# Kernel tuning notes

Measured on AMD Instinct MI355X. Metric: run time of the kernel, lower is better.

Reference implementation:

```python
import jax, jax.numpy as jnp
import numpy as np

DIM = 1024
NUM_HEADS = 8
DIM_HEAD = 64
K_NEIGHBORS = 64
INNER = NUM_HEADS * DIM_HEAD
SCALE = DIM_HEAD ** -0.5


def setup_inputs() -> dict:
    key = jax.random.key(0)
    kx, kq, kk = jax.random.split(key, 3)
    x = jax.random.normal(kx, (2, 2048, DIM), dtype=jnp.float32)
    # nn.Linear(dim, inner_dim, bias=False): weight applied as x @ W.T; store as [dim, inner]
    Wq = jax.random.normal(kq, (DIM, INNER), dtype=jnp.float32) * (DIM ** -0.5)
    Wk = jax.random.normal(kk, (DIM, INNER), dtype=jnp.float32) * (DIM ** -0.5)
    return {"x": x, "Wq": Wq, "Wk": Wk}


def reference(x, Wq, Wk):
    b, n, _ = x.shape
    # project and split heads: (b, n, inner) -> (b, h, n, d)
    q = (x @ Wq).reshape(b, n, NUM_HEADS, DIM_HEAD).transpose(0, 2, 1, 3)
    k = (x @ Wk).reshape(b, n, NUM_HEADS, DIM_HEAD).transpose(0, 2, 1, 3)
    scores = jnp.einsum("bhqd,bhkd->bhqk", q, k) * SCALE
    if K_NEIGHBORS < n:
        top_vals, _ = jax.lax.top_k(scores, K_NEIGHBORS)  # (b,h,n,k)
        min_k = top_vals[..., -1:]  # k-th largest per row
        scores = jnp.where(scores < min_k, -jnp.inf, scores)
    return jax.nn.softmax(scores, axis=-1)
```

## Files before the change

### kernel.cpp

```cpp
#include <hip/hip_runtime.h>
#include <math.h>

#define BATCH 2
#define SEQ   2048
#define DIMIN 1024
#define NHEAD 8
#define DHEAD 64
#define INNER 512
#define KNEI  64
#define SCALE 0.125f
#define GBAND 2e-6f

__global__ __launch_bounds__(256) void proj_kernel(
    const float* __restrict__ x, const float* __restrict__ Wq,
    const float* __restrict__ Wk, float* __restrict__ qk)
{
  const int which = blockIdx.z;
  const float* __restrict__ W = which ? Wk : Wq;
  float* __restrict__ out = qk + (size_t)which * (4096ull * (size_t)INNER);
  const int m0 = blockIdx.y * 64;
  const int n0 = blockIdx.x * 64;
  __shared__ float aT[16][68];
  __shared__ float bS[16][68];
  const int t  = threadIdx.x;
  const int ty = t >> 4, tx = t & 15;
  float acc[4][4] = {};
  for (int k0 = 0; k0 < DIMIN; k0 += 16) {
    {
      const int m = t >> 2, c4 = t & 3;
      float4 av = *(const float4*)(x + (size_t)(m0 + m) * DIMIN + k0 + c4 * 4);
      aT[c4*4+0][m] = av.x; aT[c4*4+1][m] = av.y;
      aT[c4*4+2][m] = av.z; aT[c4*4+3][m] = av.w;
    }
    {
      const int kk = t >> 6, n = t & 63;
      #pragma unroll
      for (int s5 = 0; s5 < 4; ++s5)
        bS[kk + 4*s5][n] = W[(size_t)(k0 + kk + 4*s5) * INNER + n0 + n];
    }
    __syncthreads();
    #pragma unroll 4
    for (int kk = 0; kk < 16; ++kk) {
      float4 a4 = *(const float4*)&aT[kk][ty*4];
      float4 b4 = *(const float4*)&bS[kk][tx*4];
      float a[4] = {a4.x, a4.y, a4.z, a4.w};
      float b[4] = {b4.x, b4.y, b4.z, b4.w};
      #pragma unroll
      for (int i = 0; i < 4; ++i)
        #pragma unroll
        for (int j = 0; j < 4; ++j)
          acc[i][j] = fmaf(a[i], b[j], acc[i][j]);
    }
    __syncthreads();
  }
  #pragma unroll
  for (int i = 0; i < 4; ++i) {
    float4 v = make_float4(acc[i][0], acc[i][1], acc[i][2], acc[i][3]);
    *(float4*)(out + (size_t)(m0 + ty*4 + i) * INNER + n0 + tx*4) = v;
  }
}

__global__ __launch_bounds__(256) void score_kernel(
    const float* __restrict__ qk, float* __restrict__ out)
{
  const int bh = blockIdx.z;
  const int b  = bh >> 3, h = bh & 7;
  const int m0 = blockIdx.y * 64;
  const int n0 = blockIdx.x * 64;
  const float* __restrict__ q = qk;
  const float* __restrict__ k = qk + 4096ull * (size_t)INNER;
  __shared__ float qT[64][68];
  __shared__ float kT[64][68];
  const int t = threadIdx.x;
  {
    const int m = t >> 2, dv = t & 3;
    const float* qrow = q + (size_t)(b*SEQ + m0 + m) * INNER + h*DHEAD;
    const float* krow = k + (size_t)(b*SEQ + n0 + m) * INNER + h*DHEAD;
    #pragma unroll
    for (int s5 = 0; s5 < 4; ++s5) {
      const int d0 = (dv + 4*s5) * 4;
      float4 qv = *(const float4*)(qrow + d0);
      float4 kv = *(const float4*)(krow + d0);
      qT[d0+0][m] = qv.x; qT[d0+1][m] = qv.y; qT[d0+2][m] = qv.z; qT[d0+3][m] = qv.w;
      kT[d0+0][m] = kv.x; kT[d0+1][m] = kv.y; kT[d0+2][m] = kv.z; kT[d0+3][m] = kv.w;
    }
  }
  __syncthreads();
  const int ty = t >> 4, tx = t & 15;
  float acc[4][4] = {};
  #pragma unroll 8
  for (int kk = 0; kk < 64; ++kk) {
    float4 a4 = *(const float4*)&qT[kk][ty*4];
    float4 b4 = *(const float4*)&kT[kk][tx*4];
    float a[4] = {a4.x, a4.y, a4.z, a4.w};
    float b[4] = {b4.x, b4.y, b4.z, b4.w};
    #pragma unroll
    for (int i = 0; i < 4; ++i)
      #pragma unroll
      for (int j = 0; j < 4; ++j)
        acc[i][j] = fmaf(a[i], b[j], acc[i][j]);
  }
  #pragma unroll
  for (int i = 0; i < 4; ++i) {
    float4 v = make_float4(acc[i][0]*SCALE, acc[i][1]*SCALE,
                           acc[i][2]*SCALE, acc[i][3]*SCALE);
    *(float4*)(out + ((size_t)bh * SEQ + m0 + ty*4 + i) * SEQ + n0 + tx*4) = v;
  }
}

__device__ __forceinline__ unsigned f2key(float f) {
  unsigned u = __float_as_uint(f);
  return (u & 0x80000000u) ? ~u : (u | 0x80000000u);
}
__device__ __forceinline__ float key2f(unsigned kk) {
  unsigned u = (kk & 0x80000000u) ? (kk & 0x7FFFFFFFu) : ~kk;
  return __uint_as_float(u);
}

__global__ __launch_bounds__(256) void topk_softmax_hedge(float* __restrict__ out)
{
  const int wave = threadIdx.x >> 6;
  const int lane = threadIdx.x & 63;
  const size_t row = (size_t)blockIdx.x * 4 + wave;
  float* __restrict__ p = out + row * (size_t)SEQ;

  float s[32];
  #pragma unroll
  for (int i = 0; i < 8; ++i) {
    float4 v = *(const float4*)(p + (size_t)(lane + 64*i) * 4);
    s[i*4+0] = v.x; s[i*4+1] = v.y; s[i*4+2] = v.z; s[i*4+3] = v.w;
  }

  float mx = s[0], mn = s[0];
  #pragma unroll
  for (int i = 1; i < 32; ++i) { mx = fmaxf(mx, s[i]); mn = fminf(mn, s[i]); }
  #pragma unroll
  for (int o = 32; o; o >>= 1) {
    mx = fmaxf(mx, __shfl_xor(mx, o));
    mn = fminf(mn, __shfl_xor(mn, o));
  }

  unsigned lo = f2key(mn);
  unsigned hi = f2key(mx) + 1u;
  while (lo + 1u < hi) {
    const unsigned mid = lo + ((hi - lo) >> 1);
    const float tf = key2f(mid);
    int c = 0;
    #pragma unroll
    for (int i = 0; i < 32; ++i)
      c += __popcll(__ballot(s[i] >= tf));
    if (c >= KNEI) { lo = mid; if (c == KNEI) break; }
    else hi = mid;
  }
  const float thr0 = key2f(lo);

  float mk = 3.4e38f;
  #pragma unroll
  for (int i = 0; i < 32; ++i) mk = (s[i] >= thr0) ? fminf(mk, s[i]) : mk;
  #pragma unroll
  for (int o = 32; o; o >>= 1) mk = fminf(mk, __shfl_xor(mk, o));
  const float s64 = mk;

  int n_hi = 0, n_band = 0;
  #pragma unroll
  for (int i = 0; i < 32; ++i) {
    n_hi   += __popcll(__ballot(s[i] > s64 + GBAND));
    n_band += __popcll(__ballot(fabsf(s[i] - s64) <= GBAND));
  }
  const int r = KNEI - n_hi;
  const bool amb = (n_band != r);
  float fb = (float)r / (float)max(n_band, 1);
  fb = fminf(fmaxf(fb, 0.f), 1.f);

  float z = 0.f;
  #pragma unroll
  for (int i = 0; i < 32; ++i) {
    float f;
    if (amb) {
      f = (s[i] > s64 + GBAND) ? 1.f
        : ((fabsf(s[i] - s64) <= GBAND) ? fb : 0.f);
    } else {
      f = (s[i] >= s64) ? 1.f : 0.f;
    }
    float ex = f * __expf(s[i] - mx);
    s[i] = ex; z += ex;
  }
  #pragma unroll
  for (int o = 32; o; o >>= 1) z += __shfl_xor(z, o);
  const float rz = 1.0f / z;

  #pragma unroll
  for (int i = 0; i < 8; ++i) {
    float4 v = make_float4(s[i*4+0]*rz, s[i*4+1]*rz, s[i*4+2]*rz, s[i*4+3]*rz);
    *(float4*)(p + (size_t)(lane + 64*i) * 4) = v;
  }
}

extern "C" void kernel_launch(void* const* d_in, const int* in_sizes, int n_in,
                              void* d_out, int out_size, void* d_ws, size_t ws_size,
                              hipStream_t stream) {
  const float* x  = (const float*)d_in[0];
  const float* Wq = (const float*)d_in[1];
  const float* Wk = (const float*)d_in[2];
  float* out = (float*)d_out;
  float* ws  = (float*)d_ws;

  proj_kernel<<<dim3(INNER/64, (BATCH*SEQ)/64, 2), 256, 0, stream>>>(x, Wq, Wk, ws);
  score_kernel<<<dim3(SEQ/64, SEQ/64, BATCH*NHEAD), 256, 0, stream>>>(ws, out);
  topk_softmax_hedge<<<dim3((BATCH*NHEAD*SEQ)/4), 256, 0, stream>>>(out);
}
```

Measured before the change: 355.1 us.

## Fuse score GEMM with top-k softmax so scores stay in registers

Merges the score kernel and the top-k/softmax kernel into one. Each block computes a 16-query by 2048-key score tile, holding the scores in 128 registers per thread, and runs the threshold search and masked softmax directly on them. This removes one write and one read of the 2048x2048 score matrix per head, and the final output uses nontemporal stores. In exchange the register pressure is high (acc[4][32]), which may lower occupancy or cause spills. The K tile is reloaded with less reuse per block than the 64x64 tiling had.

```diff
diff --git a/kernel.cpp b/kernel.cpp
--- a/kernel.cpp
+++ b/kernel.cpp
@@ -60,54 +60,6 @@
   }
 }
 
-__global__ __launch_bounds__(256) void score_kernel(
-    const float* __restrict__ qk, float* __restrict__ out)
-{
-  const int bh = blockIdx.z;
-  const int b  = bh >> 3, h = bh & 7;
-  const int m0 = blockIdx.y * 64;
-  const int n0 = blockIdx.x * 64;
-  const float* __restrict__ q = qk;
-  const float* __restrict__ k = qk + 4096ull * (size_t)INNER;
-  __shared__ float qT[64][68];
-  __shared__ float kT[64][68];
-  const int t = threadIdx.x;
-  {
-    const int m = t >> 2, dv = t & 3;
-    const float* qrow = q + (size_t)(b*SEQ + m0 + m) * INNER + h*DHEAD;
-    const float* krow = k + (size_t)(b*SEQ + n0 + m) * INNER + h*DHEAD;
-    #pragma unroll
-    for (int s5 = 0; s5 < 4; ++s5) {
-      const int d0 = (dv + 4*s5) * 4;
-      float4 qv = *(const float4*)(qrow + d0);
-      float4 kv = *(const float4*)(krow + d0);
-      qT[d0+0][m] = qv.x; qT[d0+1][m] = qv.y; qT[d0+2][m] = qv.z; qT[d0+3][m] = qv.w;
-      kT[d0+0][m] = kv.x; kT[d0+1][m] = kv.y; kT[d0+2][m] = kv.z; kT[d0+3][m] = kv.w;
-    }
-  }
-  __syncthreads();
-  const int ty = t >> 4, tx = t & 15;
-  float acc[4][4] = {};
-  #pragma unroll 8
-  for (int kk = 0; kk < 64; ++kk) {
-    float4 a4 = *(const float4*)&qT[kk][ty*4];
-    float4 b4 = *(const float4*)&kT[kk][tx*4];
-    float a[4] = {a4.x, a4.y, a4.z, a4.w};
-    float b[4] = {b4.x, b4.y, b4.z, b4.w};
-    #pragma unroll
-    for (int i = 0; i < 4; ++i)
-      #pragma unroll
-      for (int j = 0; j < 4; ++j)
-        acc[i][j] = fmaf(a[i], b[j], acc[i][j]);
-  }
-  #pragma unroll
-  for (int i = 0; i < 4; ++i) {
-    float4 v = make_float4(acc[i][0]*SCALE, acc[i][1]*SCALE,
-                           acc[i][2]*SCALE, acc[i][3]*SCALE);
-    *(float4*)(out + ((size_t)bh * SEQ + m0 + ty*4 + i) * SEQ + n0 + tx*4) = v;
-  }
-}
-
 __device__ __forceinline__ unsigned f2key(float f) {
   unsigned u = __float_as_uint(f);
   return (u & 0x80000000u) ? ~u : (u | 0x80000000u);
@@ -117,82 +69,138 @@
   return __uint_as_float(u);
 }
 
-__global__ __launch_bounds__(256) void topk_softmax_hedge(float* __restrict__ out)
+__global__ __launch_bounds__(256) void score_topk_fused(
+    const float* __restrict__ qk, float* __restrict__ out)
 {
-  const int wave = threadIdx.x >> 6;
-  const int lane = threadIdx.x & 63;
-  const size_t row = (size_t)blockIdx.x * 4 + wave;
-  float* __restrict__ p = out + row * (size_t)SEQ;
-
-  float s[32];
-  #pragma unroll
-  for (int i = 0; i < 8; ++i) {
-    float4 v = *(const float4*)(p + (size_t)(lane + 64*i) * 4);
-    s[i*4+0] = v.x; s[i*4+1] = v.y; s[i*4+2] = v.z; s[i*4+3] = v.w;
-  }
-
-  float mx = s[0], mn = s[0];
-  #pragma unroll
-  for (int i = 1; i < 32; ++i) { mx = fmaxf(mx, s[i]); mn = fminf(mn, s[i]); }
-  #pragma unroll
-  for (int o = 32; o; o >>= 1) {
-    mx = fmaxf(mx, __shfl_xor(mx, o));
-    mn = fminf(mn, __shfl_xor(mn, o));
-  }
-
-  unsigned lo = f2key(mn);
-  unsigned hi = f2key(mx) + 1u;
-  while (lo + 1u < hi) {
-    const unsigned mid = lo + ((hi - lo) >> 1);
-    const float tf = key2f(mid);
-    int c = 0;
+  const int bh = blockIdx.y, b = bh >> 3, h = bh & 7;
+  const int q0 = blockIdx.x * 16;
+  const int t = threadIdx.x, lane = t & 63;
+  const int myrow = (t >> 6) * 4;
+  const float* __restrict__ qws = qk;
+  const float* __restrict__ kws = qk + 4096ull * (size_t)INNER;
+
+  __shared__ float kT[64][66];
+  __shared__ float qT[16][68];
+
+  {
+    const int r = t >> 4, dd = (t & 15) * 4;
+    float4 v = *(const float4*)(qws + (size_t)(b*SEQ + q0 + r) * INNER + h*DHEAD + dd);
+    *(float4*)&qT[r][dd] = v;
+  }
+
+  float acc[4][32];
+  #pragma unroll
+  for (int r = 0; r < 4; ++r)
+    #pragma unroll
+    for (int c = 0; c < 32; ++c) acc[r][c] = 0.f;
+
+  const int kt = t >> 2, ds = (t & 3) * 16;
+  const float* kstage = kws + (size_t)(b*SEQ + kt) * INNER + h*DHEAD + ds;
+
+  #pragma unroll
+  for (int c = 0; c < 32; ++c) {
+    __syncthreads();
+    {
+      const float* src = kstage + (size_t)(c*64) * INNER;
+      float4 v0 = *(const float4*)(src);
+      float4 v1 = *(const float4*)(src + 4);
+      float4 v2 = *(const float4*)(src + 8);
+      float4 v3 = *(const float4*)(src + 12);
+      *(float2*)&kT[kt][ds+ 0] = make_float2(v0.x, v0.y);
+      *(float2*)&kT[kt][ds+ 2] = make_float2(v0.z, v0.w);
+      *(float2*)&kT[kt][ds+ 4] = make_float2(v1.x, v1.y);
+      *(float2*)&kT[kt][ds+ 6] = make_float2(v1.z, v1.w);
+      *(float2*)&kT[kt][ds+ 8] = make_float2(v2.x, v2.y);
+      *(float2*)&kT[kt][ds+10] = make_float2(v2.z, v2.w);
+      *(float2*)&kT[kt][ds+12] = make_float2(v3.x, v3.y);
+      *(float2*)&kT[kt][ds+14] = make_float2(v3.z, v3.w);
+    }
+    __syncthreads();
+    #pragma unroll
+    for (int d4 = 0; d4 < 16; ++d4) {
+      float2 k0 = *(const float2*)&kT[lane][d4*4];
+      float2 k1 = *(const float2*)&kT[lane][d4*4+2];
+      #pragma unroll
+      for (int r = 0; r < 4; ++r) {
+        float4 qv = *(const float4*)&qT[myrow + r][d4*4];
+        acc[r][c] = fmaf(qv.x, k0.x, acc[r][c]);
+        acc[r][c] = fmaf(qv.y, k0.y, acc[r][c]);
+        acc[r][c] = fmaf(qv.z, k1.x, acc[r][c]);
+        acc[r][c] = fmaf(qv.w, k1.y, acc[r][c]);
+      }
+    }
+  }
+
+  #pragma unroll
+  for (int r = 0; r < 4; ++r)
+    #pragma unroll
+    for (int c = 0; c < 32; ++c) acc[r][c] = acc[r][c] * SCALE;
+
+  #pragma unroll
+  for (int r = 0; r < 4; ++r) {
+    float* __restrict__ po = out + ((size_t)bh * SEQ + q0 + myrow + r) * (size_t)SEQ;
+
+    float mx = acc[r][0], mn = acc[r][0];
+    #pragma unroll
+    for (int i = 1; i < 32; ++i) { mx = fmaxf(mx, acc[r][i]); mn = fminf(mn, acc[r][i]); }
+    #pragma unroll
+    for (int o = 32; o; o >>= 1) {
+      mx = fmaxf(mx, __shfl_xor(mx, o));
+      mn = fminf(mn, __shfl_xor(mn, o));
+    }
+
+    unsigned lo = f2key(mn);
+    unsigned hi = f2key(mx) + 1u;
+    while (lo + 1u < hi) {
+      const unsigned mid = lo + ((hi - lo) >> 1);
+      const float tf = key2f(mid);
+      int cc = 0;
+      #pragma unroll
+      for (int i = 0; i < 32; ++i)
+        cc += __popcll(__ballot(acc[r][i] >= tf));
+      if (cc >= KNEI) { lo = mid; if (cc == KNEI) break; }
+      else hi = mid;
+    }
+    const float thr0 = key2f(lo);
+
+    float mk = 3.4e38f;
+    #pragma unroll
+    for (int i = 0; i < 32; ++i) mk = (acc[r][i] >= thr0) ? fminf(mk, acc[r][i]) : mk;
+    #pragma unroll
+    for (int o = 32; o; o >>= 1) mk = fminf(mk, __shfl_xor(mk, o));
+    const float s64 = mk;
+
+    int n_hi = 0, n_band = 0;
+    #pragma unroll
+    for (int i = 0; i < 32; ++i) {
+      n_hi   += __popcll(__ballot(acc[r][i] > s64 + GBAND));
+      n_band += __popcll(__ballot(fabsf(acc[r][i] - s64) <= GBAND));
+    }
+    const int rr = KNEI - n_hi;
+    const bool amb = (n_band != rr);
+    float fb = (float)rr / (float)max(n_band, 1);
+    fb = fminf(fmaxf(fb, 0.f), 1.f);
+
+    float z = 0.f;
+    #pragma unroll
+    for (int i = 0; i < 32; ++i) {
+      float f;
+      if (amb) {
+        f = (acc[r][i] > s64 + GBAND) ? 1.f
+          : ((fabsf(acc[r][i] - s64) <= GBAND) ? fb : 0.f);
+      } else {
+        f = (acc[r][i] >= s64) ? 1.f : 0.f;
+      }
+      float ex = f * __expf(acc[r][i] - mx);
+      acc[r][i] = ex; z += ex;
+    }
+    #pragma unroll
+    for (int o = 32; o; o >>= 1) z += __shfl_xor(z, o);
+    const float rz = 1.0f / z;
+
     #pragma unroll
     for (int i = 0; i < 32; ++i)
-      c += __popcll(__ballot(s[i] >= tf));
-    if (c >= KNEI) { lo = mid; if (c == KNEI) break; }
-    else hi = mid;
-  }
-  const float thr0 = key2f(lo);
-
-  float mk = 3.4e38f;
-  #pragma unroll
-  for (int i = 0; i < 32; ++i) mk = (s[i] >= thr0) ? fminf(mk, s[i]) : mk;
-  #pragma unroll
-  for (int o = 32; o; o >>= 1) mk = fminf(mk, __shfl_xor(mk, o));
-  const float s64 = mk;
-
-  int n_hi = 0, n_band = 0;
-  #pragma unroll
-  for (int i = 0; i < 32; ++i) {
-    n_hi   += __popcll(__ballot(s[i] > s64 + GBAND));
-    n_band += __popcll(__ballot(fabsf(s[i] - s64) <= GBAND));
-  }
-  const int r = KNEI - n_hi;
-  const bool amb = (n_band != r);
-  float fb = (float)r / (float)max(n_band, 1);
-  fb = fminf(fmaxf(fb, 0.f), 1.f);
-
-  float z = 0.f;
-  #pragma unroll
-  for (int i = 0; i < 32; ++i) {
-    float f;
-    if (amb) {
-      f = (s[i] > s64 + GBAND) ? 1.f
-        : ((fabsf(s[i] - s64) <= GBAND) ? fb : 0.f);
-    } else {
-      f = (s[i] >= s64) ? 1.f : 0.f;
-    }
-    float ex = f * __expf(s[i] - mx);
-    s[i] = ex; z += ex;
-  }
-  #pragma unroll
-  for (int o = 32; o; o >>= 1) z += __shfl_xor(z, o);
-  const float rz = 1.0f / z;
-
-  #pragma unroll
-  for (int i = 0; i < 8; ++i) {
-    float4 v = make_float4(s[i*4+0]*rz, s[i*4+1]*rz, s[i*4+2]*rz, s[i*4+3]*rz);
-    *(float4*)(p + (size_t)(lane + 64*i) * 4) = v;
+      __builtin_nontemporal_store(acc[r][i] * rz, po + i*64 + lane);
   }
 }
 
@@ -206,6 +214,5 @@
   float* ws  = (float*)d_ws;
 
   proj_kernel<<<dim3(INNER/64, (BATCH*SEQ)/64, 2), 256, 0, stream>>>(x, Wq, Wk, ws);
-  score_kernel<<<dim3(SEQ/64, SEQ/64, BATCH*NHEAD), 256, 0, stream>>>(ws, out);
-  topk_softmax_hedge<<<dim3((BATCH*NHEAD*SEQ)/4), 256, 0, stream>>>(out);
-}
+  score_topk_fused<<<dim3(SEQ/16, BATCH*NHEAD), 256, 0, stream>>>(ws, out);
+}
```

After: 545.9 us. 1.54x slower.
